# Optimization experiments

Hardware: AMD Instinct MI355X
Metric: run time of the kernel (lower is better)

The kernel has to match this reference:

```python
import jax, jax.numpy as jnp
import numpy as np

B, D, H = 32768, 688, 4
DH = D // H          # 172 head dim (d_model // h, overrides ctor d_k)
MH = 128             # mlp hidden
EPS = 1e-5
SCALE = 1.0 / float(np.sqrt(DH))


def _ln(x, g, b):
    m = jnp.mean(x, -1, keepdims=True)
    v = jnp.var(x, -1, keepdims=True)  # biased var, matches torch LayerNorm
    return (x - m) / jnp.sqrt(v + EPS) * g + b


def setup_inputs() -> dict:
    key = jax.random.key(0)
    ks = jax.random.split(key, 16)
    w = lambda k, o, i: jax.random.normal(k, (o, i), jnp.float32) * 0.001  # init.normal_(std=0.001)
    z = lambda n: jnp.zeros((n,), jnp.float32)
    o = lambda n: jnp.ones((n,), jnp.float32)
    return dict(
        x=jax.random.normal(ks[0], (B, D), jnp.float32),
        x2=jax.random.normal(ks[1], (B, D), jnp.float32),
        Wq_v=w(ks[2], D, D), bq_v=z(D),
        Wk_v=w(ks[3], D, D), bk_v=z(D),
        Wv_v=w(ks[4], D, D), bv_v=z(D),
        Wq_i=w(ks[5], D, D), bq_i=z(D),
        Wk_i=w(ks[6], D, D), bk_i=z(D),
        Wv_i=w(ks[7], D, D), bv_i=z(D),
        Wo_v=w(ks[8], D, D), bo_v=z(D),
        Wo_i=w(ks[9], D, D), bo_i=z(D),
        ln1_g=o(D), ln1_b=z(D), ln2_g=o(D), ln2_b=z(D),
        ln3_g=o(D), ln3_b=z(D), ln4_g=o(D), ln4_b=z(D),
        m1v_W=w(ks[10], MH, D), m1v_b=z(MH),
        m2v_W=w(ks[11], D, MH), m2v_b=z(D),
        m1i_W=w(ks[12], MH, D), m1i_b=z(MH),
        m2i_W=w(ks[13], D, MH), m2i_b=z(D),
        coef=o(8),  # LearnableCoefficient 1..8, all init to 1.0
    )


def reference(x, x2,
              Wq_v, bq_v, Wk_v, bk_v, Wv_v, bv_v,
              Wq_i, bq_i, Wk_i, bk_i, Wv_i, bv_i,
              Wo_v, bo_v, Wo_i, bo_i,
              ln1_g, ln1_b, ln2_g, ln2_b, ln3_g, ln3_b, ln4_g, ln4_b,
              m1v_W, m1v_b, m2v_W, m2v_b, m1i_W, m1i_b, m2i_W, m2i_b,
              coef):
    rgb = _ln(x, ln1_g, ln1_b)
    ir = _ln(x2, ln2_g, ln2_b)
    proj = lambda t, W, b: (t @ W.T + b).reshape(-1, H, DH)  # (B, h, d_k)
    q_vis, k_vis, v_vis = proj(rgb, Wq_v, bq_v), proj(rgb, Wk_v, bk_v), proj(rgb, Wv_v, bv_v)
    q_ir, k_ir, v_ir = proj(ir, Wq_i, bq_i), proj(ir, Wk_i, bk_i), proj(ir, Wv_i, bv_i)
    # cross attention over heads: scores are (B, h, h)
    att_vis = jax.nn.softmax(jnp.einsum('bhd,bgd->bhg', q_ir, k_vis) * SCALE, -1)
    att_ir = jax.nn.softmax(jnp.einsum('bhd,bgd->bhg', q_vis, k_ir) * SCALE, -1)
    out_vis = jnp.einsum('bhg,bgd->bhd', att_vis, v_vis).reshape(-1, D) @ Wo_v.T + bo_v
    out_ir = jnp.einsum('bhg,bgd->bhd', att_ir, v_ir).reshape(-1, D) @ Wo_i.T + bo_i
    out_vis = coef[0] * x + coef[1] * out_vis
    out_ir = coef[2] * x2 + coef[3] * out_ir
    mv = jax.nn.gelu(_ln(out_vis, ln3_g, ln3_b) @ m1v_W.T + m1v_b, approximate=False) @ m2v_W.T + m2v_b
    mi = jax.nn.gelu(_ln(out_ir, ln4_g, ln4_b) @ m1i_W.T + m1i_b, approximate=False) @ m2i_W.T + m2i_b
    out_vis = coef[4] * out_vis + coef[5] * mv
    out_ir = coef[6] * out_ir + coef[7] * mi
    return out_vis, out_ir
```

## Files before the change

kernel.cpp:

```cpp
#include <hip/hip_runtime.h>
#include <cmath>


#define B_ROWS 32768
#define D_DIM  688
#define DP     704
#define DH_DIM 172
#define MH_DIM 128

typedef unsigned short ushort_t;
typedef unsigned char  u8;
typedef __attribute__((ext_vector_type(8))) __bf16 bf16x8;
typedef __attribute__((ext_vector_type(4))) float  f32x4;

__device__ __forceinline__ float b2f(ushort_t u) {
    return __builtin_bit_cast(float, (unsigned int)u << 16);
}
__device__ __forceinline__ ushort_t f2bf(float f) {
    unsigned int u = __builtin_bit_cast(unsigned int, f);
    u += 0x7FFFu + ((u >> 16) & 1u);
    return (ushort_t)(u >> 16);
}
__device__ __forceinline__ unsigned int pk4fp8(float a, float b, float c, float d) {
    int v = 0;
    v = __builtin_amdgcn_cvt_pk_fp8_f32(a, b, v, false);
    v = __builtin_amdgcn_cvt_pk_fp8_f32(c, d, v, true);
    return (unsigned int)v;
}
__device__ __forceinline__ u8 f2fp8(float a) {
    return (u8)(__builtin_amdgcn_cvt_pk_fp8_f32(a, 0.f, 0, false) & 0xff);
}

__device__ __forceinline__ void gl2lds16(const void* g, void* l) {
    __builtin_amdgcn_global_load_lds(
        (const __attribute__((address_space(1))) unsigned int*)g,
        (__attribute__((address_space(3))) unsigned int*)l, 16, 0, 0);
}

struct CvtJobs {
    const float* src[12];
    u8*          dst[12];
    int O[12], Opad[12], Kin[12], KpadB[12];
    int isfp8[12];
    int bstart[13];
};

__global__ __launch_bounds__(256)
void cvt_all(CvtJobs jobs)
{
    int b = blockIdx.x;
    int j = 0;
    while (b >= jobs.bstart[j + 1]) ++j;
    const int t = (b - jobs.bstart[j]) * 256 + threadIdx.x;
    const int KpadB = jobs.KpadB[j];
    const int Kin   = jobs.Kin[j];
    const int cpr   = KpadB >> 4;
    if (t >= jobs.Opad[j] * cpr) return;
    const int o = t / cpr;
    const int c = t - o * cpr;
    uint4 out = make_uint4(0, 0, 0, 0);
    if (jobs.isfp8[j]) {
        if (o < jobs.O[j] && (c * 16 + 16) <= Kin) {
            const float4* s = reinterpret_cast<const float4*>(jobs.src[j] + (size_t)o * Kin + c * 16);
            float4 f0 = s[0], f1 = s[1], f2 = s[2], f3 = s[3];
            out.x = pk4fp8(f0.x, f0.y, f0.z, f0.w);
            out.y = pk4fp8(f1.x, f1.y, f1.z, f1.w);
            out.z = pk4fp8(f2.x, f2.y, f2.z, f2.w);
            out.w = pk4fp8(f3.x, f3.y, f3.z, f3.w);
        }
    } else {
        if (o < jobs.O[j] && (c * 8 + 8) <= Kin) {
            const float4* s = reinterpret_cast<const float4*>(jobs.src[j] + (size_t)o * Kin + c * 8);
            float4 f0 = s[0], f1 = s[1];
            out.x = f2bf(f0.x) | ((unsigned int)f2bf(f0.y) << 16);
            out.y = f2bf(f0.z) | ((unsigned int)f2bf(f0.w) << 16);
            out.z = f2bf(f1.x) | ((unsigned int)f2bf(f1.y) << 16);
            out.w = f2bf(f1.z) | ((unsigned int)f2bf(f1.w) << 16);
        }
    }
    *reinterpret_cast<uint4*>(jobs.dst[j] + (size_t)o * KpadB + c * 16) = out;
}

__global__ __launch_bounds__(256)
void pack_bias(const float* __restrict__ a0, const float* __restrict__ a1,
               const float* __restrict__ a2, const float* __restrict__ b0,
               const float* __restrict__ b1, const float* __restrict__ b2,
               float* __restrict__ dv, float* __restrict__ di)
{
    int t = blockIdx.x * 256 + threadIdx.x;
    if (t >= 2064) return;
    float v, w;
    if (t < 688)       { v = a0[t];        w = b0[t]; }
    else if (t < 1376) { v = a1[t - 688];  w = b1[t - 688]; }
    else               { v = a2[t - 1376]; w = b2[t - 1376]; }
    dv[t] = v; di[t] = w;
}

__global__ __launch_bounds__(256)
void ln_kernel(const float* __restrict__ Xv, const float* __restrict__ Xi,
               const float* __restrict__ gv, const float* __restrict__ bv,
               const float* __restrict__ gi, const float* __restrict__ bi,
               u8* __restrict__ Yv, u8* __restrict__ Yi)
{
    const int lane = threadIdx.x & 63;
    const int wave = threadIdx.x >> 6;
    const long w = (long)blockIdx.x * 4 + wave;
    const float* X; const float* g; const float* b; u8* Y; long r;
    if (w < B_ROWS) { X = Xv; g = gv; b = bv; Y = Yv; r = w; }
    else            { X = Xi; g = gi; b = bi; Y = Yi; r = w - B_ROWS; }

    const float4* row = reinterpret_cast<const float4*>(X + r * D_DIM);
    float4 v0 = row[lane];
    float4 v1 = row[lane + 64];
    float4 v2 = make_float4(0.f, 0.f, 0.f, 0.f);
    if (lane < 44) v2 = row[lane + 128];

    float s  = v0.x + v0.y + v0.z + v0.w + v1.x + v1.y + v1.z + v1.w
             + v2.x + v2.y + v2.z + v2.w;
    float s2 = v0.x*v0.x + v0.y*v0.y + v0.z*v0.z + v0.w*v0.w
             + v1.x*v1.x + v1.y*v1.y + v1.z*v1.z + v1.w*v1.w
             + v2.x*v2.x + v2.y*v2.y + v2.z*v2.z + v2.w*v2.w;
#pragma unroll
    for (int m = 32; m; m >>= 1) { s += __shfl_xor(s, m); s2 += __shfl_xor(s2, m); }

    const float mean = s * (1.f / 688.f);
    const float var  = s2 * (1.f / 688.f) - mean * mean;
    const float rstd = rsqrtf(var + 1e-5f);

    const float4* g4 = reinterpret_cast<const float4*>(g);
    const float4* b4 = reinterpret_cast<const float4*>(b);
    unsigned int* out32 = reinterpret_cast<unsigned int*>(Y + (size_t)r * DP);

    {
        float4 gg = g4[lane], bb = b4[lane];
        out32[lane] = pk4fp8((v0.x - mean) * rstd * gg.x + bb.x,
                             (v0.y - mean) * rstd * gg.y + bb.y,
                             (v0.z - mean) * rstd * gg.z + bb.z,
                             (v0.w - mean) * rstd * gg.w + bb.w);
    }
    {
        float4 gg = g4[lane + 64], bb = b4[lane + 64];
        out32[lane + 64] = pk4fp8((v1.x - mean) * rstd * gg.x + bb.x,
                                  (v1.y - mean) * rstd * gg.y + bb.y,
                                  (v1.z - mean) * rstd * gg.z + bb.z,
                                  (v1.w - mean) * rstd * gg.w + bb.w);
    }
    if (lane < 44) {
        float4 gg = g4[lane + 128], bb = b4[lane + 128];
        out32[lane + 128] = pk4fp8((v2.x - mean) * rstd * gg.x + bb.x,
                                   (v2.y - mean) * rstd * gg.y + bb.y,
                                   (v2.z - mean) * rstd * gg.z + bb.z,
                                   (v2.w - mean) * rstd * gg.w + bb.w);
    } else if (lane < 48) {
        out32[lane + 128] = 0u;
    }
}

template<int MODE>
__global__ __launch_bounds__(256, 2)
void gemmT(const u8* __restrict__ A0, const u8* __restrict__ A1,
           const u8* __restrict__ W0, const u8* __restrict__ W1,
           const float* __restrict__ bias0, const float* __restrict__ bias1,
           ushort_t* __restrict__ out0, ushort_t* __restrict__ out1,
           const float* __restrict__ res0, const float* __restrict__ res1,
           const float* __restrict__ coef, int ca0, int cb0, int ca1, int cb1,
           int NBn, int N, int K, int lda, int ldw, int ldo)
{
    __shared__ __align__(16) u8 lds[73728];

    const int q8 = gridDim.x >> 3;
    const int v  = (blockIdx.x & 7) * q8 + (blockIdx.x >> 3);
    const int nb = v % NBn;
    const int tmp = v / NBn;
    const int mb = tmp & 127;
    const int zz = tmp >> 7;

    const u8* A = zz ? A1 : A0;
    const u8* W = zz ? W1 : W0;
    const float* bias = zz ? bias1 : bias0;
    ushort_t* outp    = zz ? out1 : out0;
    const float* resid = zz ? res1 : res0;
    const int ca = zz ? ca1 : ca0;
    const int cb = zz ? cb1 : cb0;

    const int tid  = threadIdx.x;
    const int lane = tid & 63;
    const int wave = tid >> 6;
    const int wrow = wave >> 1;
    const int wcol = wave & 1;
    const int m0 = mb * 256;
    const int n0 = nb * 128;
    const int rl16 = lane & 15;
    const int q4   = lane >> 4;

    const int r0a  = (wave * 64 + lane) >> 2;
    const int swzk = ((lane & 3) ^ ((lane >> 3) & 3)) * 16;

    f32x4 acc[8][4];
#pragma unroll
    for (int i = 0; i < 8; ++i)
#pragma unroll
        for (int j = 0; j < 4; ++j)
            acc[i][j] = f32x4{0.f, 0.f, 0.f, 0.f};

    const int NT = K >> 6;

#define STAGET(kt, bb) do {                                                        \
    const u8* _a = A + (size_t)(m0 + r0a) * lda + (kt)*64 + swzk;                  \
    gl2lds16(_a,                     lds + (bb)*24576 + wave*1024);                \
    gl2lds16(_a +  64*(size_t)lda,   lds + (bb)*24576 + 4096 + wave*1024);         \
    gl2lds16(_a + 128*(size_t)lda,   lds + (bb)*24576 + 8192 + wave*1024);         \
    gl2lds16(_a + 192*(size_t)lda,   lds + (bb)*24576 + 12288 + wave*1024);        \
    const u8* _b = W + (size_t)(n0 + r0a) * ldw + (kt)*64 + swzk;                  \
    gl2lds16(_b,                     lds + (bb)*24576 + 16384 + wave*1024);        \
    gl2lds16(_b +  64*(size_t)ldw,   lds + (bb)*24576 + 20480 + wave*1024);        \
} while (0)

#define RDFRAG(bb) do {                                                            \
    _Pragma("unroll")                                                              \
    for (int kk = 0; kk < 2; ++kk) {                                               \
        const int bo = kk * 32 + q4 * 8;                                           \
        const int ch = bo >> 4, sb = bo & 15;                                      \
        _Pragma("unroll")                                                          \
        for (int i = 0; i < 8; ++i) {                                              \
            const int row_ = wrow * 128 + i * 16 + rl16;                           \
            af[kk][i] = *reinterpret_cast<const long*>(                            \
                lds + (bb) * 24576 + row_ * 64 + (((ch ^ ((row_ >> 1) & 3)) << 4) | sb)); \
        }                                                                          \
        _Pragma("unroll")                                                          \
        for (int j = 0; j < 4; ++j) {                                              \
            const int row_ = wcol * 64 + j * 16 + rl16;                            \
            bw[kk][j] = *reinterpret_cast<const long*>(                            \
                lds + (bb) * 24576 + 16384 + row_ * 64 + (((ch ^ ((row_ >> 1) & 3)) << 4) | sb)); \
        }                                                                          \
    } } while (0)

    long af[2][8], bw[2][4];

    STAGET(0, 0);
    STAGET(1, 1);
    asm volatile("s_waitcnt vmcnt(6)" ::: "memory");
    __builtin_amdgcn_s_barrier();
    RDFRAG(0);

    for (int t = 0; t < NT; ++t) {
        const int tn2 = (t + 2 < NT) ? t + 2 : NT - 1;
        STAGET(tn2, (t + 2) % 3);
        asm volatile("s_waitcnt vmcnt(6)" ::: "memory");
        asm volatile("s_waitcnt lgkmcnt(0)" ::: "memory");
        __builtin_amdgcn_s_barrier();
        __builtin_amdgcn_s_setprio(1);
#pragma unroll
        for (int kk = 0; kk < 2; ++kk)
#pragma unroll
            for (int i = 0; i < 8; ++i)
#pragma unroll
                for (int j = 0; j < 4; ++j)
                    acc[i][j] = __builtin_amdgcn_mfma_f32_16x16x32_fp8_fp8(
                        af[kk][i], bw[kk][j], acc[i][j], 0, 0, 0);
        __builtin_amdgcn_s_setprio(0);
        if (t + 1 < NT) RDFRAG((t + 1) % 3);
    }

    __syncthreads();

    ushort_t* const Cl = reinterpret_cast<ushort_t*>(lds);
#pragma unroll
    for (int mi = 0; mi < 8; ++mi)
#pragma unroll
        for (int nj = 0; nj < 4; ++nj)
#pragma unroll
            for (int r = 0; r < 4; ++r) {
                const int row  = wrow * 128 + mi * 16 + q4 * 4 + r;
                const int colL = wcol * 64 + nj * 16 + rl16;
                const int blk  = (colL >> 3) ^ (((row >> 2) & 3) << 1);
                Cl[row * 128 + blk * 8 + (colL & 7)] = f2bf(acc[mi][nj][r]);
            }
    __syncthreads();

    float cA = 0.f, cB = 1.f;
    if constexpr (MODE == 1) { cA = coef[ca]; cB = coef[cb]; }
#pragma unroll
    for (int it2 = 0; it2 < 16; ++it2) {
        const int c   = it2 * 256 + tid;
        const int row = c >> 4;
        const int lb  = c & 15;
        const int gcol = n0 + lb * 8;
        if (gcol >= N) continue;
        const int pb = lb ^ (((row >> 2) & 3) << 1);
        uint4 pv = *reinterpret_cast<const uint4*>(Cl + row * 128 + pb * 8);
        const ushort_t* pu = (const ushort_t*)&pv;
        float4 b0 = *reinterpret_cast<const float4*>(bias + gcol);
        float4 b1 = *reinterpret_cast<const float4*>(bias + gcol + 4);
        const float bb[8] = {b0.x, b0.y, b0.z, b0.w, b1.x, b1.y, b1.z, b1.w};
        const size_t idx = (size_t)(m0 + row) * ldo + gcol;
        ushort_t o[8];
        if constexpr (MODE == 0) {
#pragma unroll
            for (int k = 0; k < 8; ++k) o[k] = f2bf(b2f(pu[k]) + bb[k]);
        } else {
            const float* rp = resid + idx;
            float4 r0_ = reinterpret_cast<const float4*>(rp)[0];
            float4 r1_ = reinterpret_cast<const float4*>(rp)[1];
            const float rr[8] = {r0_.x, r0_.y, r0_.z, r0_.w, r1_.x, r1_.y, r1_.z, r1_.w};
#pragma unroll
            for (int k = 0; k < 8; ++k)
                o[k] = f2bf(cA * rr[k] + cB * (b2f(pu[k]) + bb[k]));
        }
        *reinterpret_cast<uint4*>(outp + idx) = *reinterpret_cast<uint4*>(o);
    }
#undef STAGET
#undef RDFRAG
}

__global__ __launch_bounds__(256)
void mlp_fused(const ushort_t* __restrict__ ov0, const ushort_t* __restrict__ ov1,
               const float* __restrict__ g0, const float* __restrict__ b0,
               const float* __restrict__ g1, const float* __restrict__ b1,
               const ushort_t* __restrict__ W10, const ushort_t* __restrict__ W11,
               const float* __restrict__ mb10, const float* __restrict__ mb11,
               const ushort_t* __restrict__ W20, const ushort_t* __restrict__ W21,
               const float* __restrict__ mb20, const float* __restrict__ mb21,
               const float* __restrict__ coef,
               float* __restrict__ out0, float* __restrict__ out1)
{
    __shared__ __align__(16) ushort_t hraw[32 * 712];
    __shared__ __align__(16) ushort_t gbuf[32 * 136];
    __shared__ float glds[704];
    __shared__ float blds[704];
    __shared__ float mlds[32];
    __shared__ float rlds[32];

    const int zz = blockIdx.y;
    const ushort_t* ovb = zz ? ov1 : ov0;
    const float* lg = zz ? g1 : g0;
    const float* lb = zz ? b1 : b0;
    const ushort_t* W1 = zz ? W11 : W10;
    const float* mb1 = zz ? mb11 : mb10;
    const ushort_t* W2 = zz ? W21 : W20;
    const float* mb2 = zz ? mb21 : mb20;
    float* outp = zz ? out1 : out0;
    const float cA = coef[zz ? 6 : 4];
    const float cB = coef[zz ? 7 : 5];

    const int tid  = threadIdx.x;
    const int lane = tid & 63;
    const int wv   = tid >> 6;
    const long r0  = (long)blockIdx.x * 32;

    if (tid < 176) {
        float4 gg = make_float4(0, 0, 0, 0), bb = make_float4(0, 0, 0, 0);
        if (tid < 172) {
            gg = reinterpret_cast<const float4*>(lg)[tid];
            bb = reinterpret_cast<const float4*>(lb)[tid];
        }
        reinterpret_cast<float4*>(glds)[tid] = gg;
        reinterpret_cast<float4*>(blds)[tid] = bb;
    }

#pragma unroll
    for (int it = 0; it < 11; ++it) {
        const int c = it * 256 + tid;
        const int row = c / 88;
        const int u = c - row * 88;
        uint4 vv = make_uint4(0, 0, 0, 0);
        if (u < 86)
            vv = *reinterpret_cast<const uint4*>(ovb + (r0 + row) * 688 + u * 8);
        *reinterpret_cast<uint4*>(&hraw[row * 712 + u * 8]) = vv;
    }
    __syncthreads();

    for (int rr = 0; rr < 8; ++rr) {
        const int row = wv * 8 + rr;
        const ushort_t* hp = &hraw[row * 712];
        ushort4 a0 = *reinterpret_cast<const ushort4*>(hp + lane * 4);
        ushort4 a1 = *reinterpret_cast<const ushort4*>(hp + 256 + lane * 4);
        ushort4 a2 = make_ushort4(0, 0, 0, 0);
        if (lane < 44) a2 = *reinterpret_cast<const ushort4*>(hp + 512 + lane * 4);
        float e[12] = {b2f(a0.x), b2f(a0.y), b2f(a0.z), b2f(a0.w),
                       b2f(a1.x), b2f(a1.y), b2f(a1.z), b2f(a1.w),
                       b2f(a2.x), b2f(a2.y), b2f(a2.z), b2f(a2.w)};
        float s = 0.f, s2 = 0.f;
#pragma unroll
        for (int k = 0; k < 12; ++k) { s += e[k]; s2 += e[k] * e[k]; }
#pragma unroll
        for (int m = 32; m; m >>= 1) { s += __shfl_xor(s, m); s2 += __shfl_xor(s2, m); }
        if (lane == 0) {
            const float mean = s * (1.f / 688.f);
            const float var  = s2 * (1.f / 688.f) - mean * mean;
            mlds[row] = mean;
            rlds[row] = rsqrtf(var + 1e-5f);
        }
    }
    __syncthreads();

#pragma unroll
    for (int it = 0; it < 11; ++it) {
        const int c = it * 256 + tid;
        if (c < 2752) {
            const int row = c / 86;
            const int u = c - row * 86;
            uint4 vv = *reinterpret_cast<const uint4*>(&hraw[row * 712 + u * 8]);
            const float mean = mlds[row], rstd = rlds[row];
            const ushort_t* pe = (const ushort_t*)&vv;
            ushort_t o[8];
#pragma unroll
            for (int k = 0; k < 8; ++k)
                o[k] = f2bf((b2f(pe[k]) - mean) * rstd * glds[u * 8 + k] + blds[u * 8 + k]);
            *reinterpret_cast<uint4*>(&hraw[row * 712 + u * 8]) = *reinterpret_cast<uint4*>(o);
        }
    }
    __syncthreads();

    const int rl16 = lane & 15;
    const int q4   = lane >> 4;

    {
        f32x4 acc[2][2];
#pragma unroll
        for (int i = 0; i < 2; ++i) { acc[i][0] = f32x4{0,0,0,0}; acc[i][1] = f32x4{0,0,0,0}; }
        for (int kt = 0; kt < 11; ++kt) {
#pragma unroll
            for (int kk = 0; kk < 64; kk += 32) {
                bf16x8 af[2], bw[2];
#pragma unroll
                for (int n = 0; n < 2; ++n)
                    bw[n] = *reinterpret_cast<const bf16x8*>(
                        W1 + (size_t)(wv * 32 + n * 16 + rl16) * 704 + kt * 64 + kk + q4 * 8);
#pragma unroll
                for (int i = 0; i < 2; ++i)
                    af[i] = *reinterpret_cast<const bf16x8*>(
                        &hraw[(i * 16 + rl16) * 712 + kt * 64 + kk + q4 * 8]);
#pragma unroll
                for (int i = 0; i < 2; ++i)
#pragma unroll
                    for (int n = 0; n < 2; ++n)
                        acc[i][n] = __builtin_amdgcn_mfma_f32_16x16x32_bf16(
                            af[i], bw[n], acc[i][n], 0, 0, 0);
            }
        }
        const int rb = q4 * 4;
#pragma unroll
        for (int n = 0; n < 2; ++n) {
            const int col = wv * 32 + n * 16 + rl16;
            const float bc = mb1[col];
#pragma unroll
            for (int i = 0; i < 2; ++i)
#pragma unroll
                for (int r = 0; r < 4; ++r) {
                    float val = acc[i][n][r] + bc;
                    val = 0.5f * val * (1.0f + erff(val * 0.70710678118654752f));
                    gbuf[(i * 16 + rb + r) * 136 + col] = f2bf(val);
                }
        }
    }
    __syncthreads();

    for (int ch = 0; ch < 11; ++ch) {
        const int col16 = wv * 176 + ch * 16;
        if (col16 >= 688) continue;
        f32x4 acc2[2];
        acc2[0] = f32x4{0, 0, 0, 0};
        acc2[1] = f32x4{0, 0, 0, 0};
#pragma unroll
        for (int kk = 0; kk < 4; ++kk) {
            bf16x8 bw2 = *reinterpret_cast<const bf16x8*>(
                W2 + (size_t)(col16 + rl16) * 128 + kk * 32 + q4 * 8);
            bf16x8 af2[2];
#pragma unroll
            for (int i = 0; i < 2; ++i)
                af2[i] = *reinterpret_cast<const bf16x8*>(
                    &gbuf[(i * 16 + rl16) * 136 + kk * 32 + q4 * 8]);
#pragma unroll
            for (int i = 0; i < 2; ++i)
                acc2[i] = __builtin_amdgcn_mfma_f32_16x16x32_bf16(af2[i], bw2, acc2[i], 0, 0, 0);
        }
        const int col = col16 + rl16;
        const float bc = mb2[col];
#pragma unroll
        for (int i = 0; i < 2; ++i)
#pragma unroll
            for (int r = 0; r < 4; ++r) {
                const long row = r0 + i * 16 + q4 * 4 + r;
                const float raw = b2f(ovb[row * 688 + col]);
                outp[row * 688 + col] = cA * raw + cB * (acc2[i][r] + bc);
            }
    }
}

__global__ __launch_bounds__(256)
void attn_kernel(const ushort_t* __restrict__ qkv_v, const ushort_t* __restrict__ qkv_i,
                 u8* __restrict__ ctx_v, u8* __restrict__ ctx_i)
{
    const int lane = threadIdx.x & 63;
    const int wave = threadIdx.x >> 6;
    const long r = (long)blockIdx.x * 4 + wave;
    const ushort_t* bv = qkv_v + r * 2064;
    const ushort_t* bi = qkv_i + r * 2064;

    float sv[4][4], si[4][4];
#pragma unroll
    for (int h = 0; h < 4; ++h)
#pragma unroll
        for (int g = 0; g < 4; ++g) { sv[h][g] = 0.f; si[h][g] = 0.f; }

    float vvr[3][4], vir[3][4];
#pragma unroll
    for (int it = 0; it < 3; ++it) {
        const int d = lane + it * 64;
        const bool ok = d < DH_DIM;
        float qv[4], kv[4], qi[4], ki[4];
#pragma unroll
        for (int h = 0; h < 4; ++h) {
            const int o = h * DH_DIM + d;
            qv[h]      = ok ? b2f(bv[o]) : 0.f;
            kv[h]      = ok ? b2f(bv[D_DIM + o]) : 0.f;
            vvr[it][h] = ok ? b2f(bv[2 * D_DIM + o]) : 0.f;
            qi[h]      = ok ? b2f(bi[o]) : 0.f;
            ki[h]      = ok ? b2f(bi[D_DIM + o]) : 0.f;
            vir[it][h] = ok ? b2f(bi[2 * D_DIM + o]) : 0.f;
        }
#pragma unroll
        for (int h = 0; h < 4; ++h)
#pragma unroll
            for (int g = 0; g < 4; ++g) {
                sv[h][g] += qi[h] * kv[g];
                si[h][g] += qv[h] * ki[g];
            }
    }

#pragma unroll
    for (int h = 0; h < 4; ++h)
#pragma unroll
        for (int g = 0; g < 4; ++g) {
            float a = sv[h][g], b = si[h][g];
#pragma unroll
            for (int m = 32; m; m >>= 1) { a += __shfl_xor(a, m); b += __shfl_xor(b, m); }
            sv[h][g] = a; si[h][g] = b;
        }

    const float scale = 0.07624928516630235f;
    float av[4][4], ai[4][4];
#pragma unroll
    for (int h = 0; h < 4; ++h) {
        float m1 = fmaxf(fmaxf(sv[h][0], sv[h][1]), fmaxf(sv[h][2], sv[h][3])) * scale;
        float m2 = fmaxf(fmaxf(si[h][0], si[h][1]), fmaxf(si[h][2], si[h][3])) * scale;
        float d1 = 0.f, d2 = 0.f;
#pragma unroll
        for (int g = 0; g < 4; ++g) {
            av[h][g] = expf(sv[h][g] * scale - m1); d1 += av[h][g];
            ai[h][g] = expf(si[h][g] * scale - m2); d2 += ai[h][g];
        }
        const float r1 = 1.f / d1, r2 = 1.f / d2;
#pragma unroll
        for (int g = 0; g < 4; ++g) { av[h][g] *= r1; ai[h][g] *= r2; }
    }

#pragma unroll
    for (int it = 0; it < 3; ++it) {
        const int d = lane + it * 64;
        if (d < DH_DIM) {
#pragma unroll
            for (int h = 0; h < 4; ++h) {
                float cv = av[h][0] * vvr[it][0] + av[h][1] * vvr[it][1]
                         + av[h][2] * vvr[it][2] + av[h][3] * vvr[it][3];
                float ci = ai[h][0] * vir[it][0] + ai[h][1] * vir[it][1]
                         + ai[h][2] * vir[it][2] + ai[h][3] * vir[it][3];
                ctx_v[r * DP + h * DH_DIM + d] = f2fp8(cv);
                ctx_i[r * DP + h * DH_DIM + d] = f2fp8(ci);
            }
        }
    }
    if (lane < 16) {
        ctx_v[r * DP + 688 + lane] = 0;
        ctx_i[r * DP + 688 + lane] = 0;
    }
}

extern "C" void kernel_launch(void* const* d_in, const int* in_sizes, int n_in,
                              void* d_out, int out_size, void* d_ws, size_t ws_size,
                              hipStream_t stream)
{
    if (n_in < 35) return;
    const float* x     = (const float*)d_in[0];
    const float* x2    = (const float*)d_in[1];
    const float* Wq_v  = (const float*)d_in[2];
    const float* bq_v  = (const float*)d_in[3];
    const float* Wk_v  = (const float*)d_in[4];
    const float* bk_v  = (const float*)d_in[5];
    const float* Wv_v  = (const float*)d_in[6];
    const float* bv_v  = (const float*)d_in[7];
    const float* Wq_i  = (const float*)d_in[8];
    const float* bq_i  = (const float*)d_in[9];
    const float* Wk_i  = (const float*)d_in[10];
    const float* bk_i  = (const float*)d_in[11];
    const float* Wv_i  = (const float*)d_in[12];
    const float* bv_i  = (const float*)d_in[13];
    const float* Wo_v  = (const float*)d_in[14];
    const float* bo_v  = (const float*)d_in[15];
    const float* Wo_i  = (const float*)d_in[16];
    const float* bo_i  = (const float*)d_in[17];
    const float* ln1_g = (const float*)d_in[18];
    const float* ln1_b = (const float*)d_in[19];
    const float* ln2_g = (const float*)d_in[20];
    const float* ln2_b = (const float*)d_in[21];
    const float* ln3_g = (const float*)d_in[22];
    const float* ln3_b = (const float*)d_in[23];
    const float* ln4_g = (const float*)d_in[24];
    const float* ln4_b = (const float*)d_in[25];
    const float* m1v_W = (const float*)d_in[26];
    const float* m1v_b = (const float*)d_in[27];
    const float* m2v_W = (const float*)d_in[28];
    const float* m2v_b = (const float*)d_in[29];
    const float* m1i_W = (const float*)d_in[30];
    const float* m1i_b = (const float*)d_in[31];
    const float* m2i_W = (const float*)d_in[32];
    const float* m2i_b = (const float*)d_in[33];
    const float* coef  = (const float*)d_in[34];

    const size_t BD = (size_t)B_ROWS * D_DIM;

    char* ws = (char*)d_ws;
    size_t off = 0;
    auto give = [&](size_t bytes) {
        char* p = ws + off;
        off += (bytes + 255) & ~(size_t)255;
        return p;
    };
    u8* Wcat_v = (u8*)give(2176ull * DP);
    u8* Wcat_i = (u8*)give(2176ull * DP);
    u8* Wo_vb  = (u8*)give(768ull * DP);
    u8* Wo_ib  = (u8*)give(768ull * DP);
    ushort_t* m1vb = (ushort_t*)give(128ull * DP * 2);
    ushort_t* m1ib = (ushort_t*)give(128ull * DP * 2);
    ushort_t* m2vb = (ushort_t*)give(768ull * 128 * 2);
    ushort_t* m2ib = (ushort_t*)give(768ull * 128 * 2);
    float* bcat_v = (float*)give(2064 * 4);
    float* bcat_i = (float*)give(2064 * 4);
    char* regX = give((size_t)B_ROWS * DP * 2);
    char* regQ = give((size_t)B_ROWS * 2064 * 2 * 2);
    if (ws_size < off) return;

    u8* xn_v  = (u8*)regX;
    u8* xn_i  = xn_v + (size_t)B_ROWS * DP;
    u8* ctx_v = xn_v;
    u8* ctx_i = xn_i;
    ushort_t* qkv_v = (ushort_t*)regQ;
    ushort_t* qkv_i = qkv_v + (size_t)B_ROWS * 2064;
    ushort_t* ovb   = (ushort_t*)regQ;
    ushort_t* oib   = ovb + BD;

    float* ov = (float*)d_out;
    float* oi = ov + BD;

    CvtJobs J;
    const float* srcs[12] = {Wq_v, Wk_v, Wv_v, Wq_i, Wk_i, Wv_i,
                             Wo_v, Wo_i, m1v_W, m1i_W, m2v_W, m2i_W};
    u8* dsts[12] = {Wcat_v, Wcat_v + 688 * DP, Wcat_v + 1376 * DP,
                    Wcat_i, Wcat_i + 688 * DP, Wcat_i + 1376 * DP,
                    Wo_vb, Wo_ib, (u8*)m1vb, (u8*)m1ib, (u8*)m2vb, (u8*)m2ib};
    int Os[12]     = {688, 688, 688, 688, 688, 688, 688, 688, 128, 128, 688, 688};
    int Opads[12]  = {688, 688, 800, 688, 688, 800, 768, 768, 128, 128, 768, 768};
    int Kins[12]   = {688, 688, 688, 688, 688, 688, 688, 688, 688, 688, 128, 128};
    int KpadBs[12] = {DP, DP, DP, DP, DP, DP, DP, DP, DP * 2, DP * 2, 256, 256};
    int fp8s[12]   = {1, 1, 1, 1, 1, 1, 1, 1, 0, 0, 0, 0};
    int bs = 0;
    for (int j = 0; j < 12; ++j) {
        J.src[j] = srcs[j]; J.dst[j] = dsts[j];
        J.O[j] = Os[j]; J.Opad[j] = Opads[j]; J.Kin[j] = Kins[j];
        J.KpadB[j] = KpadBs[j]; J.isfp8[j] = fp8s[j];
        J.bstart[j] = bs;
        bs += (Opads[j] * (KpadBs[j] >> 4) + 255) / 256;
    }
    J.bstart[12] = bs;
    cvt_all<<<dim3(bs), dim3(256), 0, stream>>>(J);

    pack_bias<<<dim3(9), dim3(256), 0, stream>>>(bq_v, bk_v, bv_v, bq_i, bk_i, bv_i,
                                                 bcat_v, bcat_i);

    ln_kernel<<<dim3(2 * B_ROWS / 4), dim3(256), 0, stream>>>(
        x, x2, ln1_g, ln1_b, ln2_g, ln2_b, xn_v, xn_i);

    gemmT<0><<<dim3(128 * 17 * 2), dim3(256), 0, stream>>>(
        xn_v, xn_i, Wcat_v, Wcat_i, bcat_v, bcat_i, qkv_v, qkv_i,
        nullptr, nullptr, nullptr, 0, 0, 0, 0, 17, 2064, 704, DP, DP, 2064);

    attn_kernel<<<dim3(B_ROWS / 4), dim3(256), 0, stream>>>(qkv_v, qkv_i, ctx_v, ctx_i);

    gemmT<1><<<dim3(128 * 6 * 2), dim3(256), 0, stream>>>(
        ctx_v, ctx_i, Wo_vb, Wo_ib, bo_v, bo_i, ovb, oib,
        x, x2, coef, 0, 1, 2, 3, 6, 688, 704, DP, DP, 688);

    mlp_fused<<<dim3(B_ROWS / 32, 2), dim3(256), 0, stream>>>(
        ovb, oib, ln3_g, ln3_b, ln4_g, ln4_b,
        m1vb, m1ib, m1v_b, m1i_b, m2vb, m2ib, m2v_b, m2i_b,
        coef, ov, oi);
}
```

Before: 587.5 us.

## Store QKV intermediates as fp8 and read 16-byte LDS fragments in GEMM

The QKV projection GEMM (MODE 0) now writes its output as packed fp8 instead of bf16, which halves the intermediate buffer. The attention kernel reads that buffer back with a software fp8-to-float decode, so QKV write and read traffic both shrink. The GEMM inner loop also loads each fragment pair as one 16-byte LDS read (longx2) instead of two 8-byte reads, and splits the MFMAs into two passes over the .x and .y halves. The cost is lower precision on Q, K and V, which could hurt accuracy, plus extra ALU work to decode each fp8 value.

```diff
diff --git a/kernel.cpp b/kernel.cpp
--- a/kernel.cpp
+++ b/kernel.cpp
@@ -12,6 +12,7 @@
 typedef unsigned char  u8;
 typedef __attribute__((ext_vector_type(8))) __bf16 bf16x8;
 typedef __attribute__((ext_vector_type(4))) float  f32x4;
+typedef __attribute__((ext_vector_type(2))) long   longx2;
 
 __device__ __forceinline__ float b2f(ushort_t u) {
     return __builtin_bit_cast(float, (unsigned int)u << 16);
@@ -29,6 +30,14 @@
 }
 __device__ __forceinline__ u8 f2fp8(float a) {
     return (u8)(__builtin_amdgcn_cvt_pk_fp8_f32(a, 0.f, 0, false) & 0xff);
+}
+__device__ __forceinline__ float fp82f(u8 b) {
+    const unsigned s = ((unsigned)b & 0x80u) << 24;
+    const unsigned e = ((unsigned)b >> 3) & 15u;
+    const unsigned m = (unsigned)b & 7u;
+    float mag = e ? __builtin_bit_cast(float, ((e + 120u) << 23) | (m << 20))
+                  : (float)m * 0.001953125f;
+    return __builtin_bit_cast(float, __builtin_bit_cast(unsigned, mag) | s);
 }
 
 __device__ __forceinline__ void gl2lds16(const void* g, void* l) {
@@ -161,7 +170,7 @@
 void gemmT(const u8* __restrict__ A0, const u8* __restrict__ A1,
            const u8* __restrict__ W0, const u8* __restrict__ W1,
            const float* __restrict__ bias0, const float* __restrict__ bias1,
-           ushort_t* __restrict__ out0, ushort_t* __restrict__ out1,
+           void* __restrict__ out0, void* __restrict__ out1,
            const float* __restrict__ res0, const float* __restrict__ res1,
            const float* __restrict__ coef, int ca0, int cb0, int ca1, int cb1,
            int NBn, int N, int K, int lda, int ldw, int ldo)
@@ -178,7 +187,7 @@
     const u8* A = zz ? A1 : A0;
     const u8* W = zz ? W1 : W0;
     const float* bias = zz ? bias1 : bias0;
-    ushort_t* outp    = zz ? out1 : out0;
+    void* outp        = zz ? out1 : out0;
     const float* resid = zz ? res1 : res0;
     const int ca = zz ? ca1 : ca0;
     const int cb = zz ? cb1 : cb0;
@@ -218,24 +227,19 @@
 
 #define RDFRAG(bb) do {                                                            \
     _Pragma("unroll")                                                              \
-    for (int kk = 0; kk < 2; ++kk) {                                               \
-        const int bo = kk * 32 + q4 * 8;                                           \
-        const int ch = bo >> 4, sb = bo & 15;                                      \
-        _Pragma("unroll")                                                          \
-        for (int i = 0; i < 8; ++i) {                                              \
-            const int row_ = wrow * 128 + i * 16 + rl16;                           \
-            af[kk][i] = *reinterpret_cast<const long*>(                            \
-                lds + (bb) * 24576 + row_ * 64 + (((ch ^ ((row_ >> 1) & 3)) << 4) | sb)); \
-        }                                                                          \
-        _Pragma("unroll")                                                          \
-        for (int j = 0; j < 4; ++j) {                                              \
-            const int row_ = wcol * 64 + j * 16 + rl16;                            \
-            bw[kk][j] = *reinterpret_cast<const long*>(                            \
-                lds + (bb) * 24576 + 16384 + row_ * 64 + (((ch ^ ((row_ >> 1) & 3)) << 4) | sb)); \
-        }                                                                          \
+    for (int i = 0; i < 8; ++i) {                                                  \
+        const int row_ = wrow * 128 + i * 16 + rl16;                               \
+        af2[i] = *reinterpret_cast<const longx2*>(                                 \
+            lds + (bb) * 24576 + row_ * 64 + ((q4 ^ ((row_ >> 1) & 3)) << 4));     \
+    }                                                                              \
+    _Pragma("unroll")                                                              \
+    for (int j = 0; j < 4; ++j) {                                                  \
+        const int row_ = wcol * 64 + j * 16 + rl16;                                \
+        bw2[j] = *reinterpret_cast<const longx2*>(                                 \
+            lds + (bb) * 24576 + 16384 + row_ * 64 + ((q4 ^ ((row_ >> 1) & 3)) << 4)); \
     } } while (0)
 
-    long af[2][8], bw[2][4];
+    longx2 af2[8], bw2[4];
 
     STAGET(0, 0);
     STAGET(1, 1);
@@ -251,13 +255,17 @@
         __builtin_amdgcn_s_barrier();
         __builtin_amdgcn_s_setprio(1);
 #pragma unroll
-        for (int kk = 0; kk < 2; ++kk)
-#pragma unroll
-            for (int i = 0; i < 8; ++i)
-#pragma unroll
-                for (int j = 0; j < 4; ++j)
-                    acc[i][j] = __builtin_amdgcn_mfma_f32_16x16x32_fp8_fp8(
-                        af[kk][i], bw[kk][j], acc[i][j], 0, 0, 0);
+        for (int i = 0; i < 8; ++i)
+#pragma unroll
+            for (int j = 0; j < 4; ++j)
+                acc[i][j] = __builtin_amdgcn_mfma_f32_16x16x32_fp8_fp8(
+                    af2[i].x, bw2[j].x, acc[i][j], 0, 0, 0);
+#pragma unroll
+        for (int i = 0; i < 8; ++i)
+#pragma unroll
+            for (int j = 0; j < 4; ++j)
+                acc[i][j] = __builtin_amdgcn_mfma_f32_16x16x32_fp8_fp8(
+                    af2[i].y, bw2[j].y, acc[i][j], 0, 0, 0);
         __builtin_amdgcn_s_setprio(0);
         if (t + 1 < NT) RDFRAG((t + 1) % 3);
     }
@@ -294,20 +302,25 @@
         float4 b1 = *reinterpret_cast<const float4*>(bias + gcol + 4);
         const float bb[8] = {b0.x, b0.y, b0.z, b0.w, b1.x, b1.y, b1.z, b1.w};
         const size_t idx = (size_t)(m0 + row) * ldo + gcol;
-        ushort_t o[8];
         if constexpr (MODE == 0) {
-#pragma unroll
-            for (int k = 0; k < 8; ++k) o[k] = f2bf(b2f(pu[k]) + bb[k]);
+            float vv[8];
+#pragma unroll
+            for (int k = 0; k < 8; ++k) vv[k] = b2f(pu[k]) + bb[k];
+            uint2 o;
+            o.x = pk4fp8(vv[0], vv[1], vv[2], vv[3]);
+            o.y = pk4fp8(vv[4], vv[5], vv[6], vv[7]);
+            *reinterpret_cast<uint2*>((u8*)outp + idx) = o;
         } else {
             const float* rp = resid + idx;
             float4 r0_ = reinterpret_cast<const float4*>(rp)[0];
             float4 r1_ = reinterpret_cast<const float4*>(rp)[1];
             const float rr[8] = {r0_.x, r0_.y, r0_.z, r0_.w, r1_.x, r1_.y, r1_.z, r1_.w};
+            ushort_t o[8];
 #pragma unroll
             for (int k = 0; k < 8; ++k)
                 o[k] = f2bf(cA * rr[k] + cB * (b2f(pu[k]) + bb[k]));
-        }
-        *reinterpret_cast<uint4*>(outp + idx) = *reinterpret_cast<uint4*>(o);
+            *reinterpret_cast<uint4*>((ushort_t*)outp + idx) = *reinterpret_cast<uint4*>(o);
+        }
     }
 #undef STAGET
 #undef RDFRAG
@@ -489,14 +502,14 @@
 }
 
 __global__ __launch_bounds__(256)
-void attn_kernel(const ushort_t* __restrict__ qkv_v, const ushort_t* __restrict__ qkv_i,
+void attn_kernel(const u8* __restrict__ qkv_v, const u8* __restrict__ qkv_i,
                  u8* __restrict__ ctx_v, u8* __restrict__ ctx_i)
 {
     const int lane = threadIdx.x & 63;
     const int wave = threadIdx.x >> 6;
     const long r = (long)blockIdx.x * 4 + wave;
-    const ushort_t* bv = qkv_v + r * 2064;
-    const ushort_t* bi = qkv_i + r * 2064;
+    const u8* bv = qkv_v + r * 2064;
+    const u8* bi = qkv_i + r * 2064;
 
     float sv[4][4], si[4][4];
 #pragma unroll
@@ -513,12 +526,12 @@
 #pragma unroll
         for (int h = 0; h < 4; ++h) {
             const int o = h * DH_DIM + d;
-            qv[h]      = ok ? b2f(bv[o]) : 0.f;
-            kv[h]      = ok ? b2f(bv[D_DIM + o]) : 0.f;
-            vvr[it][h] = ok ? b2f(bv[2 * D_DIM + o]) : 0.f;
-            qi[h]      = ok ? b2f(bi[o]) : 0.f;
-            ki[h]      = ok ? b2f(bi[D_DIM + o]) : 0.f;
-            vir[it][h] = ok ? b2f(bi[2 * D_DIM + o]) : 0.f;
+            qv[h]      = ok ? fp82f(bv[o]) : 0.f;
+            kv[h]      = ok ? fp82f(bv[D_DIM + o]) : 0.f;
+            vvr[it][h] = ok ? fp82f(bv[2 * D_DIM + o]) : 0.f;
+            qi[h]      = ok ? fp82f(bi[o]) : 0.f;
+            ki[h]      = ok ? fp82f(bi[D_DIM + o]) : 0.f;
+            vir[it][h] = ok ? fp82f(bi[2 * D_DIM + o]) : 0.f;
         }
 #pragma unroll
         for (int h = 0; h < 4; ++h)
@@ -638,17 +651,17 @@
     float* bcat_v = (float*)give(2064 * 4);
     float* bcat_i = (float*)give(2064 * 4);
     char* regX = give((size_t)B_ROWS * DP * 2);
-    char* regQ = give((size_t)B_ROWS * 2064 * 2 * 2);
+    char* regQ = give((size_t)B_ROWS * 2064 * 2);
     if (ws_size < off) return;
 
     u8* xn_v  = (u8*)regX;
     u8* xn_i  = xn_v + (size_t)B_ROWS * DP;
     u8* ctx_v = xn_v;
     u8* ctx_i = xn_i;
-    ushort_t* qkv_v = (ushort_t*)regQ;
-    ushort_t* qkv_i = qkv_v + (size_t)B_ROWS * 2064;
-    ushort_t* ovb   = (ushort_t*)regQ;
-    ushort_t* oib   = ovb + BD;
+    u8* qkv_v = (u8*)regQ;
+    u8* qkv_i = qkv_v + (size_t)B_ROWS * 2064;
+    ushort_t* ovb = (ushort_t*)regQ;
+    ushort_t* oib = ovb + BD;
 
     float* ov = (float*)d_out;
     float* oi = ov + BD;
```

Result: slower. 691.4 us (+17.7%).
